# Performance work log

Measured on AMD Instinct MI355X. Metric: run time of the kernel, lower is better.

## Reference

```python
import math
import jax, jax.numpy as jnp
import numpy as np

B, L, S, H, E, D = 2, 2048, 2048, 16, 64, 64

def setup_inputs() -> dict:
    key = jax.random.key(0)
    k1, k2, k3, k4, k5 = jax.random.split(key, 5)
    return {
        "queries": jax.random.normal(k1, (B, L, H, E), dtype=jnp.float32),
        "keys": jax.random.normal(k2, (B, S, H, E), dtype=jnp.float32),
        "values": jax.random.normal(k3, (B, S, H, D), dtype=jnp.float32),
        "tau": jax.random.uniform(k4, (B, 1), dtype=jnp.float32),
        "delta": jax.random.normal(k5, (B, S), dtype=jnp.float32),
        "attn_mask": jnp.zeros((1,), dtype=jnp.bool_),
    }

def reference(queries, keys, values, tau, delta, attn_mask):
    # queries: [B,L,H,E], keys: [B,S,H,E], values: [B,S,H,D]
    # tau: [B,1] -> [B,1,1,1]; delta: [B,S] -> [B,1,1,S]
    # mask_flag=False, so attn_mask is unused. Dropout is identity at eval.
    E_ = queries.shape[-1]
    scale = 1.0 / math.sqrt(E_)
    scores = jnp.einsum('blhe,bshe->bhls', queries, keys)  # [B,H,L,S]
    scores = scores * tau[:, None, None, :]                # de-stationary scale
    scores = scores + delta[:, None, None, :]              # de-stationary shift
    A = jax.nn.softmax(scale * scores, axis=-1)            # [B,H,L,S]
    V = jnp.einsum('bhls,bshd->blhd', A, values)           # [B,L,H,D]
    return V
```

## Files before the change

kernel.cpp:

```cpp
#include <hip/hip_runtime.h>


#define Bb 2
#define Ll 2048
#define Ss 2048
#define Hh 16
#define Ee 64
#define Dd 64
#define KV 64

typedef _Float16 f16x8 __attribute__((ext_vector_type(8)));
typedef _Float16 f16x4 __attribute__((ext_vector_type(4)));
typedef __fp16 fp16x2 __attribute__((ext_vector_type(2)));
typedef float f32x4 __attribute__((ext_vector_type(4)));

union Pk2 { fp16x2 h; unsigned u; };
union PackU { unsigned u[4]; f16x8 v; };

#define GLDS(gp, lp) __builtin_amdgcn_global_load_lds( \
    (const __attribute__((address_space(1))) void*)(gp), \
    (__attribute__((address_space(3))) void*)(lp), 16, 0, 0)

__global__ __launch_bounds__(256)
void prepass_k(const float* __restrict__ K, _Float16* __restrict__ K16)
{
    const unsigned v = blockIdx.x * 256 + threadIdx.x;
    const unsigned e4 = v & 15;
    const unsigned h  = (v >> 4) & 15;
    const unsigned s  = (v >> 8) & (Ss - 1);
    const unsigned b  = v >> 19;
    const f32x4 src = ((const f32x4*)K)[v];
    f16x4 t;
    t[0] = (_Float16)src[0]; t[1] = (_Float16)src[1];
    t[2] = (_Float16)src[2]; t[3] = (_Float16)src[3];
    ((f16x4*)K16)[(((size_t)(b * Hh + h) * Ss + s) * 16) + e4] = t;
}

__global__ __launch_bounds__(256)
void prepass_v(const float* __restrict__ V, _Float16* __restrict__ VT16)
{
    __shared__ _Float16 TL[64][66];
    const int tid  = threadIdx.x;
    const int wave = tid >> 6;
    const int lane = tid & 63;
    const int bh = blockIdx.y;
    const int b  = bh >> 4;
    const int h  = bh & 15;
    const int s0 = blockIdx.x * 64;

    #pragma unroll
    for (int rr = 0; rr < 16; ++rr) {
        const int row = wave * 16 + rr;
        TL[row][lane] = (_Float16)V[((size_t)(b * Ss + s0 + row) * Hh + h) * Dd + lane];
    }
    __syncthreads();
    const int d  = tid >> 2;
    const int sq = (tid & 3) * 16;
    union { _Float16 h[16]; f16x8 v[2]; } tmp;
    #pragma unroll
    for (int i = 0; i < 16; ++i) tmp.h[i] = TL[sq + i][d];
    f16x8* dp = (f16x8*)(VT16 + ((size_t)(b * Hh + h) * Dd + d) * Ss + s0 + sq);
    dp[0] = tmp.v[0];
    dp[1] = tmp.v[1];
}

__global__ __launch_bounds__(256)
void dsattn_fwd_v2(const float* __restrict__ Q, const _Float16* __restrict__ K16,
                   const _Float16* __restrict__ VT16, const float* __restrict__ tau,
                   const float* __restrict__ delta, float* __restrict__ out)
{
    __shared__ __align__(16) unsigned char Ksm[KV * 128];
    __shared__ __align__(16) unsigned char Vsm[64 * 128];
    __shared__ float dsm[KV];
    __shared__ float Osm[4][16][68];

    const int tid  = threadIdx.x;
    const int wave = tid >> 6;
    const int lane = tid & 63;
    const int lq   = lane & 15;
    const int g    = lane >> 4;

    const int bh = blockIdx.y;
    const int b  = bh >> 4;
    const int h  = bh & 15;
    const int q0 = blockIdx.x * 64;

    const float alpha = 0.125f * tau[b];

    f16x8 aq[2];
    {
        const float* qp = Q + (((size_t)b * Ll + q0 + wave * 16 + lq) * Hh + h) * Ee;
        #pragma unroll
        for (int es = 0; es < 2; ++es) {
            const float* p = qp + es * 32 + g * 8;
            f16x8 t;
            #pragma unroll
            for (int j = 0; j < 8; ++j) t[j] = (_Float16)p[j];
            aq[es] = t;
        }
    }

    f32x4 osum[4];
    #pragma unroll
    for (int i = 0; i < 4; ++i) osum[i] = (f32x4){0.f, 0.f, 0.f, 0.f};
    float m_run = -1e30f, l_run = 0.0f;

    const unsigned char* kb  = (const unsigned char*)(K16 + (size_t)(b * Hh + h) * Ss * Ee);
    const unsigned char* vtb = (const unsigned char*)(VT16 + (size_t)(b * Hh + h) * Dd * Ss);
    const float* db = delta + (size_t)b * Ss;

    const int row0  = tid >> 3;
    const int slotS = (tid & 7) ^ (row0 & 7);
    unsigned char* ksm_w = Ksm + wave * 1024;
    unsigned char* vsm_w = Vsm + wave * 1024;

    for (int sb = 0; sb < Ss; sb += KV) {
        __syncthreads();
        GLDS(kb + (size_t)(sb + row0) * 128 + slotS * 16,        ksm_w);
        GLDS(kb + (size_t)(sb + row0 + 32) * 128 + slotS * 16,   ksm_w + 4096);
        GLDS(vtb + (size_t)row0 * (Ss * 2) + sb * 2 + slotS * 16,        vsm_w);
        GLDS(vtb + (size_t)(row0 + 32) * (Ss * 2) + sb * 2 + slotS * 16, vsm_w + 4096);
        if (tid < KV) dsm[tid] = 0.125f * db[sb + tid];
        __syncthreads();

        float p[16];
        float tmax = -1e30f;
        #pragma unroll
        for (int t = 0; t < 4; ++t) {
            f32x4 c = (f32x4){0.f, 0.f, 0.f, 0.f};
            const int srow = t * 16 + lq;
            #pragma unroll
            for (int es = 0; es < 2; ++es) {
                const int slot = (es * 4 + g) ^ (srow & 7);
                f16x8 ak = *(const f16x8*)(Ksm + srow * 128 + slot * 16);
                c = __builtin_amdgcn_mfma_f32_16x16x32_f16(ak, aq[es], c, 0, 0, 0);
            }
            #pragma unroll
            for (int j = 0; j < 4; ++j) {
                float z = alpha * c[j] + dsm[t * 16 + 4 * g + j];
                p[t * 4 + j] = z;
                tmax = fmaxf(tmax, z);
            }
        }
        tmax = fmaxf(tmax, __shfl_xor(tmax, 16));
        tmax = fmaxf(tmax, __shfl_xor(tmax, 32));
        const float m_new = fmaxf(m_run, tmax);
        const float corr  = __expf(m_run - m_new);
        float psum = 0.f;
        #pragma unroll
        for (int i = 0; i < 16; ++i) { p[i] = __expf(p[i] - m_new); psum += p[i]; }
        psum += __shfl_xor(psum, 16);
        psum += __shfl_xor(psum, 32);
        l_run = l_run * corr + psum;
        m_run = m_new;
        #pragma unroll
        for (int dt = 0; dt < 4; ++dt)
            #pragma unroll
            for (int j = 0; j < 4; ++j)
                osum[dt][j] *= corr;

        unsigned pk[8];
        #pragma unroll
        for (int t = 0; t < 4; ++t) {
            Pk2 u0, u1;
            u0.h = __builtin_amdgcn_cvt_pkrtz(p[4 * t], p[4 * t + 1]);
            u1.h = __builtin_amdgcn_cvt_pkrtz(p[4 * t + 2], p[4 * t + 3]);
            pk[t * 2] = u0.u;
            pk[t * 2 + 1] = u1.u;
        }
        const int srcA = lq + 32 * (g & 1);
        const int srcB = srcA + 16;
        const bool gh = (g >> 1);
        PackU bp[2];
        #pragma unroll
        for (int ks = 0; ks < 2; ++ks) {
            unsigned a0 = __shfl(pk[ks * 4 + 0], srcA), a1 = __shfl(pk[ks * 4 + 1], srcA);
            unsigned a2 = __shfl(pk[ks * 4 + 2], srcA), a3 = __shfl(pk[ks * 4 + 3], srcA);
            unsigned b0 = __shfl(pk[ks * 4 + 0], srcB), b1 = __shfl(pk[ks * 4 + 1], srcB);
            unsigned b2 = __shfl(pk[ks * 4 + 2], srcB), b3 = __shfl(pk[ks * 4 + 3], srcB);
            bp[ks].u[0] = gh ? a2 : a0;
            bp[ks].u[1] = gh ? a3 : a1;
            bp[ks].u[2] = gh ? b2 : b0;
            bp[ks].u[3] = gh ? b3 : b1;
        }

        #pragma unroll
        for (int ks = 0; ks < 2; ++ks)
            #pragma unroll
            for (int dt = 0; dt < 4; ++dt) {
                const int vrow = dt * 16 + lq;
                const int slot = (ks * 4 + g) ^ (vrow & 7);
                f16x8 av = *(const f16x8*)(Vsm + vrow * 128 + slot * 16);
                osum[dt] = __builtin_amdgcn_mfma_f32_16x16x32_f16(av, bp[ks].v, osum[dt], 0, 0, 0);
            }
    }

    const float inv = 1.0f / l_run;
    #pragma unroll
    for (int dt = 0; dt < 4; ++dt)
        #pragma unroll
        for (int j = 0; j < 4; ++j)
            Osm[wave][lq][dt * 16 + 4 * g + j] = osum[dt][j] * inv;
    __syncthreads();
    {
        float* ob = out + (((size_t)b * Ll + q0 + wave * 16) * Hh + h) * Dd;
        #pragma unroll
        for (int r = 0; r < 16; ++r)
            ob[(size_t)r * (Hh * Dd) + lane] = Osm[wave][r][lane];
    }
}

__global__ __launch_bounds__(256)
void dsattn_fwd(const float* __restrict__ Q, const float* __restrict__ K,
                const float* __restrict__ V, const float* __restrict__ tau,
                const float* __restrict__ delta, float* __restrict__ out)
{
    __shared__ __align__(16) unsigned char Ksm[32 * 128];
    __shared__ __align__(16) unsigned char VTsm[64 * 80];
    __shared__ float dsm[32];
    __shared__ float Osm[4][16][68];

    const int tid  = threadIdx.x;
    const int wave = tid >> 6;
    const int lane = tid & 63;
    const int lq   = lane & 15;
    const int g    = lane >> 4;

    const int bh = blockIdx.y;
    const int b  = bh >> 4;
    const int h  = bh & 15;
    const int q0 = blockIdx.x * 64;

    const float alpha = 0.125f * tau[b];

    f16x8 aq[2];
    {
        const float* qp = Q + (((long)b * Ll + q0 + wave * 16 + lq) * Hh + h) * Ee;
        #pragma unroll
        for (int es = 0; es < 2; ++es) {
            const float* p = qp + es * 32 + g * 8;
            f16x8 t;
            #pragma unroll
            for (int j = 0; j < 8; ++j) t[j] = (_Float16)p[j];
            aq[es] = t;
        }
    }

    f32x4 osum[4];
    #pragma unroll
    for (int i = 0; i < 4; ++i) osum[i] = (f32x4){0.f, 0.f, 0.f, 0.f};
    float m_run = -1e30f, l_run = 0.0f;

    const float* kb = K + ((long)b * Ss * Hh + h) * Ee;
    const float* vb = V + ((long)b * Ss * Hh + h) * Dd;
    const float* db = delta + (long)b * Ss;

    const int kr    = tid >> 3;
    const int kc    = (tid & 7) * 8;
    const int kslot = (((tid & 7) ^ (kr & 7)) * 16);
    const int vd    = tid & 63;
    const int vsh   = tid >> 6;

    for (int sb = 0; sb < Ss; sb += 32) {
        __syncthreads();
        {
            const float* src = kb + (long)(sb + kr) * (Hh * Ee) + kc;
            f16x8 t;
            #pragma unroll
            for (int j = 0; j < 8; ++j) t[j] = (_Float16)src[j];
            *(f16x8*)(Ksm + kr * 128 + kslot) = t;
        }
        {
            const float* src = vb + (long)(sb + vsh * 8) * (Hh * Dd) + vd;
            f16x8 t;
            #pragma unroll
            for (int j = 0; j < 8; ++j) t[j] = (_Float16)src[j * (Hh * Dd)];
            *(f16x8*)(VTsm + vd * 80 + vsh * 16) = t;
        }
        if (tid < 32) dsm[tid] = 0.125f * db[sb + tid];
        __syncthreads();

        float p[8];
        float tmax = -1e30f;
        #pragma unroll
        for (int t = 0; t < 2; ++t) {
            f32x4 c = (f32x4){0.f, 0.f, 0.f, 0.f};
            #pragma unroll
            for (int es = 0; es < 2; ++es) {
                const int srow = t * 16 + lq;
                const int slot = ((es * 4 + g) ^ (srow & 7)) * 16;
                f16x8 ak = *(const f16x8*)(Ksm + srow * 128 + slot);
                c = __builtin_amdgcn_mfma_f32_16x16x32_f16(ak, aq[es], c, 0, 0, 0);
            }
            #pragma unroll
            for (int j = 0; j < 4; ++j) {
                float z = alpha * c[j] + dsm[t * 16 + 4 * g + j];
                p[t * 4 + j] = z;
                tmax = fmaxf(tmax, z);
            }
        }
        tmax = fmaxf(tmax, __shfl_xor(tmax, 16));
        tmax = fmaxf(tmax, __shfl_xor(tmax, 32));
        const float m_new = fmaxf(m_run, tmax);
        const float corr  = __expf(m_run - m_new);
        float psum = 0.f;
        #pragma unroll
        for (int i = 0; i < 8; ++i) { p[i] = __expf(p[i] - m_new); psum += p[i]; }
        psum += __shfl_xor(psum, 16);
        psum += __shfl_xor(psum, 32);
        l_run = l_run * corr + psum;
        m_run = m_new;
        #pragma unroll
        for (int dt = 0; dt < 4; ++dt)
            #pragma unroll
            for (int j = 0; j < 4; ++j)
                osum[dt][j] *= corr;

        Pk2 u00, u01, u10, u11;
        u00.h = __builtin_amdgcn_cvt_pkrtz(p[0], p[1]);
        u01.h = __builtin_amdgcn_cvt_pkrtz(p[2], p[3]);
        u10.h = __builtin_amdgcn_cvt_pkrtz(p[4], p[5]);
        u11.h = __builtin_amdgcn_cvt_pkrtz(p[6], p[7]);
        const int srcA = lq + 32 * (g & 1);
        const int srcB = srcA + 16;
        unsigned a00 = __shfl(u00.u, srcA), a01 = __shfl(u01.u, srcA);
        unsigned a10 = __shfl(u10.u, srcA), a11 = __shfl(u11.u, srcA);
        unsigned b00 = __shfl(u00.u, srcB), b01 = __shfl(u01.u, srcB);
        unsigned b10 = __shfl(u10.u, srcB), b11 = __shfl(u11.u, srcB);
        const bool hi = (g >= 2);
        PackU bp;
        bp.u[0] = hi ? a10 : a00;
        bp.u[1] = hi ? a11 : a01;
        bp.u[2] = hi ? b10 : b00;
        bp.u[3] = hi ? b11 : b01;

        #pragma unroll
        for (int dt = 0; dt < 4; ++dt) {
            f16x8 av = *(const f16x8*)(VTsm + (dt * 16 + lq) * 80 + g * 16);
            osum[dt] = __builtin_amdgcn_mfma_f32_16x16x32_f16(av, bp.v, osum[dt], 0, 0, 0);
        }
    }

    const float inv = 1.0f / l_run;
    #pragma unroll
    for (int dt = 0; dt < 4; ++dt)
        #pragma unroll
        for (int j = 0; j < 4; ++j)
            Osm[wave][lq][dt * 16 + 4 * g + j] = osum[dt][j] * inv;
    __syncthreads();
    {
        float* ob = out + (((long)b * Ll + q0 + wave * 16) * Hh + h) * Dd;
        #pragma unroll
        for (int r = 0; r < 16; ++r)
            ob[(long)r * (Hh * Dd) + lane] = Osm[wave][r][lane];
    }
}

extern "C" void kernel_launch(void* const* d_in, const int* in_sizes, int n_in,
                              void* d_out, int out_size, void* d_ws, size_t ws_size,
                              hipStream_t stream) {
    const float* Q     = (const float*)d_in[0];
    const float* K     = (const float*)d_in[1];
    const float* V     = (const float*)d_in[2];
    const float* tau   = (const float*)d_in[3];
    const float* delta = (const float*)d_in[4];
    float* out = (float*)d_out;

    const size_t elems = (size_t)Bb * Hh * Ss * Ee;
    const size_t need  = elems * 2 * 2;
    dim3 grid(Ll / 64, Bb * Hh);

    if (ws_size >= need) {
        _Float16* K16  = (_Float16*)d_ws;
        _Float16* VT16 = K16 + elems;
        hipLaunchKernelGGL(prepass_k, dim3(elems / 4 / 256), dim3(256), 0, stream, K, K16);
        hipLaunchKernelGGL(prepass_v, dim3(Ss / 64, Bb * Hh), dim3(256), 0, stream, V, VT16);
        hipLaunchKernelGGL(dsattn_fwd_v2, grid, dim3(256), 0, stream, Q, K16, VT16, tau, delta, out);
    } else {
        hipLaunchKernelGGL(dsattn_fwd, grid, dim3(256), 0, stream, Q, K, V, tau, delta, out);
    }
}
```

Before: 98.99 us.

## Double-buffer K/V tiles, prefetch delta in registers, add lazy softmax rescale

```diff
diff --git a/kernel.cpp b/kernel.cpp
--- a/kernel.cpp
+++ b/kernel.cpp
@@ -22,7 +22,8 @@
     (__attribute__((address_space(3))) void*)(lp), 16, 0, 0)
 
 __global__ __launch_bounds__(256)
-void prepass_k(const float* __restrict__ K, _Float16* __restrict__ K16)
+void prepass_k(const float* __restrict__ K, _Float16* __restrict__ K16,
+               const float* __restrict__ delta, float* __restrict__ delta2)
 {
     const unsigned v = blockIdx.x * 256 + threadIdx.x;
     const unsigned e4 = v & 15;
@@ -34,6 +35,11 @@
     t[0] = (_Float16)src[0]; t[1] = (_Float16)src[1];
     t[2] = (_Float16)src[2]; t[3] = (_Float16)src[3];
     ((f16x4*)K16)[(((size_t)(b * Hh + h) * Ss + s) * 16) + e4] = t;
+    if (v < (Bb * Ss) / 4) {
+        f32x4 dd = ((const f32x4*)delta)[v];
+        ((f32x4*)delta2)[v] = (f32x4){0.125f * dd[0], 0.125f * dd[1],
+                                      0.125f * dd[2], 0.125f * dd[3]};
+    }
 }
 
 __global__ __launch_bounds__(256)
@@ -65,14 +71,11 @@
 }
 
 __global__ __launch_bounds__(256)
-void dsattn_fwd_v2(const float* __restrict__ Q, const _Float16* __restrict__ K16,
+void dsattn_fwd_v3(const float* __restrict__ Q, const _Float16* __restrict__ K16,
                    const _Float16* __restrict__ VT16, const float* __restrict__ tau,
-                   const float* __restrict__ delta, float* __restrict__ out)
+                   const float* __restrict__ delta2, float* __restrict__ out)
 {
-    __shared__ __align__(16) unsigned char Ksm[KV * 128];
-    __shared__ __align__(16) unsigned char Vsm[64 * 128];
-    __shared__ float dsm[KV];
-    __shared__ float Osm[4][16][68];
+    extern __shared__ __align__(16) unsigned char smem[];
 
     const int tid  = threadIdx.x;
     const int wave = tid >> 6;
@@ -107,24 +110,51 @@
 
     const unsigned char* kb  = (const unsigned char*)(K16 + (size_t)(b * Hh + h) * Ss * Ee);
     const unsigned char* vtb = (const unsigned char*)(VT16 + (size_t)(b * Hh + h) * Dd * Ss);
-    const float* db = delta + (size_t)b * Ss;
+    const float* d2b = delta2 + (size_t)b * Ss;
 
     const int row0  = tid >> 3;
     const int slotS = (tid & 7) ^ (row0 & 7);
-    unsigned char* ksm_w = Ksm + wave * 1024;
-    unsigned char* vsm_w = Vsm + wave * 1024;
-
+
+    {
+        unsigned char* kw = smem + wave * 1024;
+        unsigned char* vw = smem + 8192 + wave * 1024;
+        GLDS(kb + (size_t)row0 * 128 + slotS * 16,        kw);
+        GLDS(kb + (size_t)(row0 + 32) * 128 + slotS * 16, kw + 4096);
+        GLDS(vtb + (size_t)row0 * (Ss * 2) + slotS * 16,        vw);
+        GLDS(vtb + (size_t)(row0 + 32) * (Ss * 2) + slotS * 16, vw + 4096);
+    }
+    f32x4 dcur[4], dnxt[4];
+    #pragma unroll
+    for (int t = 0; t < 4; ++t)
+        dcur[t] = *(const f32x4*)(d2b + t * 16 + 4 * g);
+    __syncthreads();
+
+    int cur = 0;
     for (int sb = 0; sb < Ss; sb += KV) {
-        __syncthreads();
-        GLDS(kb + (size_t)(sb + row0) * 128 + slotS * 16,        ksm_w);
-        GLDS(kb + (size_t)(sb + row0 + 32) * 128 + slotS * 16,   ksm_w + 4096);
-        GLDS(vtb + (size_t)row0 * (Ss * 2) + sb * 2 + slotS * 16,        vsm_w);
-        GLDS(vtb + (size_t)(row0 + 32) * (Ss * 2) + sb * 2 + slotS * 16, vsm_w + 4096);
-        if (tid < KV) dsm[tid] = 0.125f * db[sb + tid];
-        __syncthreads();
+        const int nb = (sb + KV < Ss);
+        if (nb) {
+            unsigned char* kw = smem + (cur ^ 1) * 16384 + wave * 1024;
+            unsigned char* vw = kw + 8192;
+            const int sn = sb + KV;
+            GLDS(kb + (size_t)(sn + row0) * 128 + slotS * 16,        kw);
+            GLDS(kb + (size_t)(sn + row0 + 32) * 128 + slotS * 16,   kw + 4096);
+            GLDS(vtb + (size_t)row0 * (Ss * 2) + sn * 2 + slotS * 16,        vw);
+            GLDS(vtb + (size_t)(row0 + 32) * (Ss * 2) + sn * 2 + slotS * 16, vw + 4096);
+        }
+        {
+            const int sn = nb ? sb + KV : sb;
+            #pragma unroll
+            for (int t = 0; t < 4; ++t)
+                dnxt[t] = *(const f32x4*)(d2b + sn + t * 16 + 4 * g);
+        }
+
+        const unsigned char* Ksm = smem + cur * 16384;
+        const unsigned char* Vsm = Ksm + 8192;
 
         float p[16];
         float tmax = -1e30f;
+        __builtin_amdgcn_s_setprio(1);
+        f32x4 c4[4];
         #pragma unroll
         for (int t = 0; t < 4; ++t) {
             f32x4 c = (f32x4){0.f, 0.f, 0.f, 0.f};
@@ -135,29 +165,37 @@
                 f16x8 ak = *(const f16x8*)(Ksm + srow * 128 + slot * 16);
                 c = __builtin_amdgcn_mfma_f32_16x16x32_f16(ak, aq[es], c, 0, 0, 0);
             }
+            c4[t] = c;
+        }
+        __builtin_amdgcn_s_setprio(0);
+        #pragma unroll
+        for (int t = 0; t < 4; ++t)
             #pragma unroll
             for (int j = 0; j < 4; ++j) {
-                float z = alpha * c[j] + dsm[t * 16 + 4 * g + j];
+                float z = fmaf(alpha, c4[t][j], dcur[t][j]);
                 p[t * 4 + j] = z;
                 tmax = fmaxf(tmax, z);
             }
-        }
+
         tmax = fmaxf(tmax, __shfl_xor(tmax, 16));
         tmax = fmaxf(tmax, __shfl_xor(tmax, 32));
-        const float m_new = fmaxf(m_run, tmax);
-        const float corr  = __expf(m_run - m_new);
+        if (!__all(tmax <= m_run + 8.0f)) {
+            const float m_new = fmaxf(m_run, tmax);
+            const float corr  = __expf(m_run - m_new);
+            l_run *= corr;
+            #pragma unroll
+            for (int dt = 0; dt < 4; ++dt)
+                #pragma unroll
+                for (int j = 0; j < 4; ++j)
+                    osum[dt][j] *= corr;
+            m_run = m_new;
+        }
         float psum = 0.f;
         #pragma unroll
-        for (int i = 0; i < 16; ++i) { p[i] = __expf(p[i] - m_new); psum += p[i]; }
+        for (int i = 0; i < 16; ++i) { p[i] = __expf(p[i] - m_run); psum += p[i]; }
         psum += __shfl_xor(psum, 16);
         psum += __shfl_xor(psum, 32);
-        l_run = l_run * corr + psum;
-        m_run = m_new;
-        #pragma unroll
-        for (int dt = 0; dt < 4; ++dt)
-            #pragma unroll
-            for (int j = 0; j < 4; ++j)
-                osum[dt][j] *= corr;
+        l_run += psum;
 
         unsigned pk[8];
         #pragma unroll
@@ -184,6 +222,7 @@
             bp[ks].u[3] = gh ? b3 : b1;
         }
 
+        __builtin_amdgcn_s_setprio(1);
         #pragma unroll
         for (int ks = 0; ks < 2; ++ks)
             #pragma unroll
@@ -193,8 +232,15 @@
                 f16x8 av = *(const f16x8*)(Vsm + vrow * 128 + slot * 16);
                 osum[dt] = __builtin_amdgcn_mfma_f32_16x16x32_f16(av, bp[ks].v, osum[dt], 0, 0, 0);
             }
-    }
-
+        __builtin_amdgcn_s_setprio(0);
+
+        __syncthreads();
+        cur ^= 1;
+        #pragma unroll
+        for (int t = 0; t < 4; ++t) dcur[t] = dnxt[t];
+    }
+
+    float (*Osm)[16][68] = (float (*)[16][68])smem;
     const float inv = 1.0f / l_run;
     #pragma unroll
     for (int dt = 0; dt < 4; ++dt)
@@ -367,15 +413,18 @@
     float* out = (float*)d_out;
 
     const size_t elems = (size_t)Bb * Hh * Ss * Ee;
-    const size_t need  = elems * 2 * 2;
+    const size_t need  = elems * 2 * 2 + (size_t)Bb * Ss * 4;
     dim3 grid(Ll / 64, Bb * Hh);
 
     if (ws_size >= need) {
-        _Float16* K16  = (_Float16*)d_ws;
-        _Float16* VT16 = K16 + elems;
-        hipLaunchKernelGGL(prepass_k, dim3(elems / 4 / 256), dim3(256), 0, stream, K, K16);
+        _Float16* K16    = (_Float16*)d_ws;
+        _Float16* VT16   = K16 + elems;
+        float*    delta2 = (float*)(VT16 + elems);
+        hipLaunchKernelGGL(prepass_k, dim3(elems / 4 / 256), dim3(256), 0, stream,
+                           K, K16, delta, delta2);
         hipLaunchKernelGGL(prepass_v, dim3(Ss / 64, Bb * Hh), dim3(256), 0, stream, V, VT16);
-        hipLaunchKernelGGL(dsattn_fwd_v2, grid, dim3(256), 0, stream, Q, K16, VT16, tau, delta, out);
+        hipLaunchKernelGGL(dsattn_fwd_v3, grid, dim3(256), 32768, stream,
+                           Q, K16, VT16, tau, delta2, out);
     } else {
         hipLaunchKernelGGL(dsattn_fwd, grid, dim3(256), 0, stream, Q, K, V, tau, delta, out);
     }
```

After: 95.96 us. 1.03x faster.
